# Optimization experiments

Measured on AMD Instinct MI355X. Metric: run time of the kernel, lower is better.

Reference implementation:

```python
import jax, jax.numpy as jnp
import numpy as np

EPS = 1e-5

def mean_variance_norm(x):
    # x: [b, c, h, w]; per-(b,c) instance norm over spatial, unbiased var (torch default)
    b, c, h, w = x.shape
    xf = x.reshape(b, c, h * w)
    mean = xf.mean(axis=2)
    var = xf.var(axis=2, ddof=1) + EPS
    std = jnp.sqrt(var)
    return (x - mean[:, :, None, None]) / std[:, :, None, None]

def conv1x1(x, w, b):
    # w: [out_c, in_c], b: [out_c]
    return jnp.einsum('oc,bchw->bohw', w, x) + b[None, :, None, None]

def setup_inputs() -> dict:
    key = jax.random.key(0)
    ks = jax.random.split(key, 10)
    b, C, H, W = 4, 512, 64, 64
    content = jax.random.normal(ks[0], (b, C, H, W), dtype=jnp.float32)
    style = jax.random.normal(ks[1], (b, C, H, W), dtype=jnp.float32)
    def w_(k, o, i):
        return jax.random.normal(k, (o, i), dtype=jnp.float32) * 0.02
    def b_(k, o):
        return jax.random.normal(k, (o,), dtype=jnp.float32) * 0.02
    return {
        'content': content, 'style': style,
        'f_w': w_(ks[2], C, C), 'f_b': b_(ks[3], C),
        'g_w': w_(ks[4], C, C), 'g_b': b_(ks[5], C),
        'h_w': w_(ks[6], C, C), 'h_b': b_(ks[7], C),
        'out_w': w_(ks[8], C, C), 'out_b': b_(ks[9], C),
    }

def reference(content, style, f_w, f_b, g_w, g_b, h_w, h_b, out_w, out_b):
    b, C, h, w = content.shape
    F = conv1x1(mean_variance_norm(content), f_w, f_b)   # [b,C,h,w]
    G = conv1x1(mean_variance_norm(style), g_w, g_b)     # [b,C,hg,wg]
    H = conv1x1(style, h_w, h_b)                          # [b,C,hg,wg]
    # spatial <= max_sample, so no subsampling branch
    Gf = G.reshape(b, C, -1)                              # [b,C,M]
    Hf = H.reshape(b, C, -1)                              # [b,C,M]
    Ff = F.reshape(b, C, -1)                              # [b,C,N]
    S = jnp.einsum('bcn,bcm->bnm', Ff, Gf)                # [b,N,M]
    S = jax.nn.softmax(S, axis=-1)
    styled = jnp.einsum('bcm,bnm->bcn', Hf, S)            # [b,C,N]
    styled = styled.reshape(b, C, h, w)
    return conv1x1(styled, out_w, out_b)
```

## Files before the change

### kernel.cpp

```cpp
#include <hip/hip_runtime.h>
#include <hip/hip_bf16.h>

typedef _Float16 f16;
typedef __attribute__((ext_vector_type(8))) _Float16 half8;
typedef __attribute__((ext_vector_type(4))) _Float16 half4;
typedef __attribute__((ext_vector_type(4))) float f32x4;

#define AS1 __attribute__((address_space(1)))
#define AS3 __attribute__((address_space(3)))

constexpr int CH  = 512;
constexpr int NSP = 4096;
constexpr int NB  = 4;

#define VM8  asm volatile("s_waitcnt vmcnt(8)"  ::: "memory")
#define VM0  asm volatile("s_waitcnt vmcnt(0)"  ::: "memory")
#define BARS do { __builtin_amdgcn_s_barrier(); asm volatile("" ::: "memory"); } while (0)

__device__ __forceinline__ void gload_lds16(const void* g, void* l) {
    __builtin_amdgcn_global_load_lds((const AS1 void*)g, (AS3 void*)l, 16, 0, 0);
}

__global__ void stats_kernel(const float* __restrict__ c_, const float* __restrict__ s_,
                             float* __restrict__ stats)
{
    int row = blockIdx.x;
    const float* p = ((row < NB*CH) ? c_ : s_) + (size_t)(row & (NB*CH - 1)) * NSP;
    float s = 0.f, ss = 0.f;
    for (int i = threadIdx.x; i < NSP/4; i += 256) {
        float4 v = ((const float4*)p)[i];
        s  += v.x + v.y + v.z + v.w;
        ss += v.x*v.x + v.y*v.y + v.z*v.z + v.w*v.w;
    }
    #pragma unroll
    for (int off = 32; off; off >>= 1) { s += __shfl_down(s, off); ss += __shfl_down(ss, off); }
    __shared__ float r1[4], r2[4];
    if ((threadIdx.x & 63) == 0) { r1[threadIdx.x >> 6] = s; r2[threadIdx.x >> 6] = ss; }
    __syncthreads();
    if (threadIdx.x == 0) {
        s = r1[0]+r1[1]+r1[2]+r1[3]; ss = r2[0]+r2[1]+r2[2]+r2[3];
        float mean = s * (1.f/NSP);
        float var  = (ss - (float)NSP*mean*mean) * (1.f/(NSP-1));
        int base = (row < NB*CH) ? 0 : 2*NB*CH;
        int r = row & (NB*CH - 1);
        stats[base + r] = mean;
        stats[base + NB*CH + r] = rsqrtf(var + 1e-5f);
    }
}

__global__ void effw_kernel(const float* __restrict__ fw, const float* __restrict__ fb,
                            const float* __restrict__ gw, const float* __restrict__ gb,
                            const float* __restrict__ hw, const float* __restrict__ ow,
                            const float* __restrict__ stats,
                            f16* __restrict__ fw_e, float* __restrict__ fb_e,
                            f16* __restrict__ gw_e, float* __restrict__ gb_e,
                            f16* __restrict__ hw_h, f16* __restrict__ ow_h)
{
    int o = blockIdx.x, b = blockIdx.y, mode = blockIdx.z, t = threadIdx.x;
    if (mode >= 2) {
        if (b != 0) return;
        const float* srcw = (mode == 2) ? hw : ow;
        f16* dstw = (mode == 2) ? hw_h : ow_h;
        for (int c = t; c < CH; c += 128) dstw[o*CH + c] = (f16)srcw[o*CH + c];
        return;
    }
    const float* w  = mode ? gw : fw;
    const float* st = stats + (mode ? 2*NB*CH : 0);
    f16* we = mode ? gw_e : fw_e;
    float part = 0.f;
    for (int c = t; c < CH; c += 128) {
        float mn = st[b*CH + c], is = st[NB*CH + b*CH + c];
        float wv = w[o*CH + c];
        we[((size_t)b*CH + o)*CH + c] = (f16)(wv * is);
        part += wv * mn * is;
    }
    #pragma unroll
    for (int off = 32; off; off >>= 1) part += __shfl_down(part, off);
    __shared__ float rr[2];
    if ((t & 63) == 0) rr[t >> 6] = part;
    __syncthreads();
    if (t == 0) (mode ? gb_e : fb_e)[b*CH + o] = (mode ? gb : fb)[o] - (rr[0] + rr[1]);
}

__global__ void transpose_f16_kernel(const float* __restrict__ content, const float* __restrict__ style,
                                     f16* __restrict__ content_t, f16* __restrict__ style_t)
{
    int b = blockIdx.z & 3, is_style = blockIdx.z >> 2;
    const float* src = (is_style ? style : content) + (size_t)b * CH * NSP;
    f16* dst = (is_style ? style_t : content_t) + (size_t)b * NSP * CH;
    int c0 = blockIdx.y * 64, n0 = blockIdx.x * 64;
    __shared__ f16 tile[64][72];
    int t = threadIdx.x;
    #pragma unroll
    for (int i = 0; i < 4; i++) {
        int idx = t + i*256;
        int cr = idx >> 4, n4 = (idx & 15) * 4;
        float4 v = *(const float4*)(src + (size_t)(c0+cr)*NSP + n0 + n4);
        tile[cr][n4+0] = (f16)v.x; tile[cr][n4+1] = (f16)v.y;
        tile[cr][n4+2] = (f16)v.z; tile[cr][n4+3] = (f16)v.w;
    }
    __syncthreads();
    int nr = t >> 2, seg = (t & 3) * 16;
    __align__(16) f16 out_v[16];
    #pragma unroll
    for (int j = 0; j < 16; j++) out_v[j] = tile[seg + j][nr];
    f16* dp = dst + (size_t)(n0+nr)*CH + c0 + seg;
    *(int4*)dp = ((int4*)out_v)[0];
    *(int4*)(dp + 8) = ((int4*)out_v)[1];
}

template<int MODE>
__global__ __launch_bounds__(256)
void gemm_kernel(const f16* __restrict__ W, long wstrideb,
                 const f16* __restrict__ Xt, long xstrideb,
                 const float* __restrict__ bias, long bstrideb,
                 void* __restrict__ Y, long ystrideb,
                 int K, long ostride)
{
    const int z = blockIdx.z;
    W    += (size_t)z * wstrideb;
    Xt   += (size_t)z * xstrideb;
    bias += (size_t)z * bstrideb;
    const int m0 = blockIdx.y * 128, n0 = blockIdx.x * 128;
    const int t = threadIdx.x, wave = t >> 6, lane = t & 63;
    const int l15 = lane & 15, l4 = lane >> 4;
    const int wm = (wave >> 1) * 64, wn = (wave & 1) * 64;

    __shared__ __align__(16) f16 Al[2][8192];
    __shared__ __align__(16) f16 Bl[2][8192];

    f32x4 acc[4][4] = {};

    auto stage = [&](int bufi, int kk) {
        #pragma unroll
        for (int j = 0; j < 4; j++) {
            int L  = ((wave*4 + j)*64 + lane) * 16;
            int SL = L ^ (((L >> 7) & 7) << 4);
            int row = SL >> 7, seg = (SL & 127) >> 1;
            gload_lds16(W  + (size_t)(m0 + row)*K + kk + seg, &Al[bufi][L >> 1]);
            gload_lds16(Xt + (size_t)(n0 + row)*K + kk + seg, &Bl[bufi][L >> 1]);
        }
    };

    const int nks = K >> 6;
    stage(0, 0);
    for (int ks = 0; ks < nks; ks++) {
        int bufi = ks & 1;
        if (ks < nks-1) { stage(bufi ^ 1, (ks + 1) * 64); VM8; }
        else            { VM0; }
        BARS;
        #pragma unroll
        for (int kb = 0; kb < 2; kb++) {
            half8 a[4], bb[4];
            #pragma unroll
            for (int i = 0; i < 4; i++) {
                int ab = (wm + i*16 + l15)*128 + kb*64 + l4*16;
                ab ^= ((ab >> 7) & 7) << 4;
                a[i] = *(const half8*)&Al[bufi][ab >> 1];
                int bby = (wn + i*16 + l15)*128 + kb*64 + l4*16;
                bby ^= ((bby >> 7) & 7) << 4;
                bb[i] = *(const half8*)&Bl[bufi][bby >> 1];
            }
            #pragma unroll
            for (int i = 0; i < 4; i++)
                #pragma unroll
                for (int jj = 0; jj < 4; jj++)
                    acc[i][jj] = __builtin_amdgcn_mfma_f32_16x16x32_f16(a[i], bb[jj], acc[i][jj], 0, 0, 0);
        }
        BARS;
    }

    #pragma unroll
    for (int i = 0; i < 4; i++) {
        const int ob = m0 + wm + i*16 + l4*4;
        f32x4 bv = *(const f32x4*)(bias + ob);
        #pragma unroll
        for (int jj = 0; jj < 4; jj++) {
            const int n = n0 + wn + jj*16 + l15;
            f32x4 v = acc[i][jj];
            v[0] += bv[0]; v[1] += bv[1]; v[2] += bv[2]; v[3] += bv[3];
            if constexpr (MODE == 0) {
                f16* Yb = (f16*)Y + (size_t)z * ystrideb;
                half4 pk; pk[0]=(f16)v[0]; pk[1]=(f16)v[1]; pk[2]=(f16)v[2]; pk[3]=(f16)v[3];
                *(half4*)(Yb + (size_t)n * ostride + ob) = pk;
            } else if constexpr (MODE == 1) {
                f16* Yb = (f16*)Y + (size_t)z * ystrideb;
                #pragma unroll
                for (int r = 0; r < 4; r++) Yb[(size_t)(ob + r) * ostride + n] = (f16)v[r];
            } else {
                float* Yf = (float*)Y + (size_t)z * ystrideb;
                #pragma unroll
                for (int r = 0; r < 4; r++) Yf[(size_t)(ob + r) * ostride + n] = v[r];
            }
        }
    }
}

__global__ __launch_bounds__(256)
void softmax_kernel(f16* __restrict__ S, int nrows)
{
    int row = blockIdx.x * 4 + (threadIdx.x >> 6);
    if (row >= nrows) return;
    int lane = threadIdx.x & 63;
    f16* p = S + (size_t)row * NSP + lane * 8;

    half8 v[8];
    #pragma unroll
    for (int j = 0; j < 8; j++) v[j] = *(const half8*)(p + j * 512);

    float mx = -1e30f;
    #pragma unroll
    for (int j = 0; j < 8; j++)
        #pragma unroll
        for (int e = 0; e < 8; e++) mx = fmaxf(mx, (float)v[j][e]);
    #pragma unroll
    for (int off = 32; off; off >>= 1) mx = fmaxf(mx, __shfl_xor(mx, off));

    float ex[64];
    float s = 0.f;
    #pragma unroll
    for (int j = 0; j < 8; j++)
        #pragma unroll
        for (int e = 0; e < 8; e++) {
            float x = __expf((float)v[j][e] - mx);
            ex[j*8 + e] = x; s += x;
        }
    #pragma unroll
    for (int off = 32; off; off >>= 1) s += __shfl_xor(s, off);
    float inv = 1.0f / s;

    #pragma unroll
    for (int j = 0; j < 8; j++) {
        half8 o;
        #pragma unroll
        for (int e = 0; e < 8; e++) o[e] = (f16)(ex[j*8 + e] * inv);
        *(half8*)(p + j * 512) = o;
    }
}

extern "C" void kernel_launch(void* const* d_in, const int* in_sizes, int n_in,
                              void* d_out, int out_size, void* d_ws, size_t ws_size,
                              hipStream_t stream)
{
    const float* content = (const float*)d_in[0];
    const float* style   = (const float*)d_in[1];
    const float* f_w = (const float*)d_in[2];
    const float* f_b = (const float*)d_in[3];
    const float* g_w = (const float*)d_in[4];
    const float* g_b = (const float*)d_in[5];
    const float* h_w = (const float*)d_in[6];
    const float* h_b = (const float*)d_in[7];
    const float* o_w = (const float*)d_in[8];
    const float* o_b = (const float*)d_in[9];

    char* ws = (char*)d_ws;
    size_t off = 0;
    auto alloc = [&](size_t bytes) -> void* {
        void* p = ws + off;
        off += (bytes + 255) & ~(size_t)255;
        return p;
    };
    float* stats = (float*)alloc(4 * NB*CH * 4);
    float* zeros = (float*)alloc(NSP * 4);
    f16* fw_e = (f16*)alloc((size_t)NB*CH*CH*2);
    f16* gw_e = (f16*)alloc((size_t)NB*CH*CH*2);
    f16* hw_h = (f16*)alloc((size_t)CH*CH*2);
    f16* ow_h = (f16*)alloc((size_t)CH*CH*2);
    float* fb_e = (float*)alloc((size_t)NB*CH*4);
    float* gb_e = (float*)alloc((size_t)NB*CH*4);
    f16* content_t = (f16*)alloc((size_t)NB*NSP*CH*2);
    f16* style_t   = (f16*)alloc((size_t)NB*NSP*CH*2);
    f16* F_t = (f16*)alloc((size_t)NB*NSP*CH*2);
    f16* G_t = (f16*)alloc((size_t)NB*NSP*CH*2);
    f16* H_  = (f16*)alloc((size_t)NB*CH*NSP*2);
    f16* styled_t = content_t;

    size_t s_plane = (size_t)NSP * NSP;
    bool all4 = (off + 4 * s_plane * 2 <= ws_size);
    f16* S16 = (f16*)alloc((all4 ? 4 : 1) * s_plane * 2);
    if (off > ws_size) return;

    hipMemsetAsync(zeros, 0, NSP * 4, stream);
    stats_kernel<<<dim3(2*NB*CH), dim3(256), 0, stream>>>(content, style, stats);
    effw_kernel<<<dim3(CH, NB, 4), dim3(128), 0, stream>>>(f_w, f_b, g_w, g_b, h_w, o_w, stats,
                                                           fw_e, fb_e, gw_e, gb_e, hw_h, ow_h);
    transpose_f16_kernel<<<dim3(NSP/64, CH/64, NB*2), dim3(256), 0, stream>>>(content, style, content_t, style_t);

    gemm_kernel<0><<<dim3(NSP/128, CH/128, NB), dim3(256), 0, stream>>>(
        fw_e, (long)CH*CH, content_t, (long)NSP*CH, fb_e, (long)CH, (void*)F_t, (long)NSP*CH, CH, (long)CH);
    gemm_kernel<0><<<dim3(NSP/128, CH/128, NB), dim3(256), 0, stream>>>(
        gw_e, (long)CH*CH, style_t, (long)NSP*CH, gb_e, (long)CH, (void*)G_t, (long)NSP*CH, CH, (long)CH);
    gemm_kernel<1><<<dim3(NSP/128, CH/128, NB), dim3(256), 0, stream>>>(
        hw_h, 0L, style_t, (long)NSP*CH, h_b, 0L, (void*)H_, (long)CH*NSP, CH, (long)NSP);

    if (all4) {
        gemm_kernel<0><<<dim3(NSP/128, NSP/128, NB), dim3(256), 0, stream>>>(
            G_t, (long)NSP*CH, F_t, (long)NSP*CH, zeros, 0L, (void*)S16, (long)s_plane, CH, (long)NSP);
        softmax_kernel<<<dim3(NB*NSP/4), dim3(256), 0, stream>>>(S16, NB*NSP);
        gemm_kernel<0><<<dim3(NSP/128, CH/128, NB), dim3(256), 0, stream>>>(
            H_, (long)CH*NSP, S16, (long)s_plane, zeros, 0L, (void*)styled_t, (long)NSP*CH, NSP, (long)CH);
    } else {
        for (int b = 0; b < NB; b++) {
            gemm_kernel<0><<<dim3(NSP/128, NSP/128, 1), dim3(256), 0, stream>>>(
                G_t + (size_t)b*NSP*CH, 0L, F_t + (size_t)b*NSP*CH, 0L, zeros, 0L,
                (void*)S16, 0L, CH, (long)NSP);
            softmax_kernel<<<dim3(NSP/4), dim3(256), 0, stream>>>(S16, NSP);
            gemm_kernel<0><<<dim3(NSP/128, CH/128, 1), dim3(256), 0, stream>>>(
                H_ + (size_t)b*CH*NSP, 0L, S16, 0L, zeros, 0L,
                (void*)(styled_t + (size_t)b*NSP*CH), 0L, NSP, (long)CH);
        }
    }

    gemm_kernel<2><<<dim3(NSP/128, CH/128, NB), dim3(256), 0, stream>>>(
        ow_h, 0L, styled_t, (long)NSP*CH, o_b, 0L, d_out, (long)CH*NSP, CH, (long)NSP);
}
```

Measured before the change: 343.7 us.

## Add 256x256-tile pipelined GEMM kernel for attention score and weighted-sum GEMMs

Adds a 512-thread GEMM kernel with 256x256 output tiles, double-buffered LDS filled by direct global-to-LDS loads, and a four-phase schedule that interleaves the next tile's loads with MFMA work using sched barriers and wave priority. It replaces the 128x128 GEMMs for the S=GᵀF product and the S·H product. The second GEMM swaps its operand roles so S becomes the M side with transposed output. The aim is more operand reuse per LDS load and better hiding of memory latency in the two largest GEMMs. In exchange it uses much more LDS and registers per block, which lowers occupancy, and the styled GEMM launches only 2 tiles along N per batch.

```diff
diff --git a/kernel.cpp b/kernel.cpp
--- a/kernel.cpp
+++ b/kernel.cpp
@@ -13,9 +13,13 @@
 constexpr int NSP = 4096;
 constexpr int NB  = 4;
 
+#define VMC2 asm volatile("s_waitcnt vmcnt(2)" ::: "memory")
 #define VM8  asm volatile("s_waitcnt vmcnt(8)"  ::: "memory")
 #define VM0  asm volatile("s_waitcnt vmcnt(0)"  ::: "memory")
 #define BARS do { __builtin_amdgcn_s_barrier(); asm volatile("" ::: "memory"); } while (0)
+#define SB0  __builtin_amdgcn_sched_barrier(0)
+#define SP1  __builtin_amdgcn_s_setprio(1)
+#define SP0  __builtin_amdgcn_s_setprio(0)
 
 __device__ __forceinline__ void gload_lds16(const void* g, void* l) {
     __builtin_amdgcn_global_load_lds((const AS1 void*)g, (AS3 void*)l, 16, 0, 0);
@@ -191,6 +195,136 @@
                 float* Yf = (float*)Y + (size_t)z * ystrideb;
                 #pragma unroll
                 for (int r = 0; r < 4; r++) Yf[(size_t)(ob + r) * ostride + n] = v[r];
+            }
+        }
+    }
+}
+
+template<int MODE>
+__global__ __launch_bounds__(512)
+void gemm256_kernel(const f16* __restrict__ W, long wstrideb,
+                    const f16* __restrict__ Xt, long xstrideb,
+                    void* __restrict__ Y, long ystrideb,
+                    int K, long ostride)
+{
+    const int z = blockIdx.z;
+    W  += (size_t)z * wstrideb;
+    Xt += (size_t)z * xstrideb;
+    const int m0 = blockIdx.y * 256, n0 = blockIdx.x * 256;
+    const int t = threadIdx.x, lane = t & 63;
+    const int wave = t >> 6;
+    const int l15 = lane & 15, l4 = lane >> 4;
+    const int wr = wave >> 2, wc = wave & 3;
+
+    __shared__ __align__(16) f16 As[2][16384];
+    __shared__ __align__(16) f16 Bs[2][16384];
+
+    f32x4 acc[8][4] = {};
+
+    auto stA = [&](int nbuf, int kk, int q) {
+        int L = q*8192 + t*16;
+        int SL = L ^ (((L >> 7) & 7) << 4);
+        gload_lds16(W + (size_t)(m0 + (SL >> 7))*K + kk + ((SL & 127) >> 1), &As[nbuf][L >> 1]);
+    };
+    auto stB = [&](int nbuf, int kk, int q) {
+        int L = q*8192 + t*16;
+        int SL = L ^ (((L >> 7) & 7) << 4);
+        gload_lds16(Xt + (size_t)(n0 + (SL >> 7))*K + kk + ((SL & 127) >> 1), &Bs[nbuf][L >> 1]);
+    };
+    auto ldA = [&](int buf, int i, int kb) {
+        int L = (wr*128 + i*16 + l15)*128 + kb*64 + l4*16;
+        L ^= ((L >> 7) & 7) << 4;
+        return *(const half8*)&As[buf][L >> 1];
+    };
+    auto ldB = [&](int buf, int j, int kb) {
+        int L = (wc*64 + j*16 + l15)*128 + kb*64 + l4*16;
+        L ^= ((L >> 7) & 7) << 4;
+        return *(const half8*)&Bs[buf][L >> 1];
+    };
+
+    const int nks = K >> 6;
+    #pragma unroll
+    for (int q = 0; q < 4; q++) stA(0, 0, q);
+    #pragma unroll
+    for (int q = 0; q < 4; q++) stB(0, 0, q);
+
+    half8 a[4][2], b01[2][2], b23[2][2];
+
+    for (int kt = 0; kt < nks; kt++) {
+        const int buf = kt & 1;
+        const bool st = (kt + 1 < nks);
+        const int kk1 = (kt + 1) << 6;
+
+        if (st) { stA(buf^1, kk1, 0); stA(buf^1, kk1, 1); VMC2; }
+        else    { VM0; }
+        BARS;
+        #pragma unroll
+        for (int i = 0; i < 4; i++) { a[i][0] = ldA(buf, i, 0); a[i][1] = ldA(buf, i, 1); }
+        #pragma unroll
+        for (int j = 0; j < 2; j++) { b01[j][0] = ldB(buf, j, 0); b01[j][1] = ldB(buf, j, 1); }
+        SB0; SP1;
+        #pragma unroll
+        for (int i = 0; i < 4; i++)
+            #pragma unroll
+            for (int j = 0; j < 2; j++)
+                #pragma unroll
+                for (int kb = 0; kb < 2; kb++)
+                    acc[i][j] = __builtin_amdgcn_mfma_f32_16x16x32_f16(a[i][kb], b01[j][kb], acc[i][j], 0, 0, 0);
+        SP0; SB0; BARS;
+
+        if (st) { stA(buf^1, kk1, 2); stA(buf^1, kk1, 3); }
+        #pragma unroll
+        for (int j = 0; j < 2; j++) { b23[j][0] = ldB(buf, 2+j, 0); b23[j][1] = ldB(buf, 2+j, 1); }
+        SB0; SP1;
+        #pragma unroll
+        for (int i = 0; i < 4; i++)
+            #pragma unroll
+            for (int j = 0; j < 2; j++)
+                #pragma unroll
+                for (int kb = 0; kb < 2; kb++)
+                    acc[i][2+j] = __builtin_amdgcn_mfma_f32_16x16x32_f16(a[i][kb], b23[j][kb], acc[i][2+j], 0, 0, 0);
+        SP0; SB0; BARS;
+
+        if (st) { stB(buf^1, kk1, 0); stB(buf^1, kk1, 1); }
+        #pragma unroll
+        for (int i = 0; i < 4; i++) { a[i][0] = ldA(buf, 4+i, 0); a[i][1] = ldA(buf, 4+i, 1); }
+        SB0; SP1;
+        #pragma unroll
+        for (int i = 0; i < 4; i++)
+            #pragma unroll
+            for (int j = 0; j < 2; j++)
+                #pragma unroll
+                for (int kb = 0; kb < 2; kb++)
+                    acc[4+i][2+j] = __builtin_amdgcn_mfma_f32_16x16x32_f16(a[i][kb], b23[j][kb], acc[4+i][2+j], 0, 0, 0);
+        SP0; SB0; BARS;
+
+        if (st) { stB(buf^1, kk1, 2); stB(buf^1, kk1, 3); }
+        SB0; SP1;
+        #pragma unroll
+        for (int i = 0; i < 4; i++)
+            #pragma unroll
+            for (int j = 0; j < 2; j++)
+                #pragma unroll
+                for (int kb = 0; kb < 2; kb++)
+                    acc[4+i][j] = __builtin_amdgcn_mfma_f32_16x16x32_f16(a[i][kb], b01[j][kb], acc[4+i][j], 0, 0, 0);
+        SP0; SB0; BARS;
+    }
+
+    #pragma unroll
+    for (int i = 0; i < 8; i++) {
+        const int ob = m0 + wr*128 + i*16 + l4*4;
+        #pragma unroll
+        for (int j = 0; j < 4; j++) {
+            const int ncol = n0 + wc*64 + j*16 + l15;
+            f32x4 v = acc[i][j];
+            if constexpr (MODE == 0) {
+                f16* Yb = (f16*)Y + (size_t)z * ystrideb;
+                half4 pk; pk[0]=(f16)v[0]; pk[1]=(f16)v[1]; pk[2]=(f16)v[2]; pk[3]=(f16)v[3];
+                *(half4*)(Yb + (size_t)ncol * ostride + ob) = pk;
+            } else {
+                f16* Yb = (f16*)Y + (size_t)z * ystrideb;
+                #pragma unroll
+                for (int r = 0; r < 4; r++) Yb[(size_t)(ob + r) * ostride + ncol] = (f16)v[r];
             }
         }
     }
@@ -294,19 +428,19 @@
         hw_h, 0L, style_t, (long)NSP*CH, h_b, 0L, (void*)H_, (long)CH*NSP, CH, (long)NSP);
 
     if (all4) {
-        gemm_kernel<0><<<dim3(NSP/128, NSP/128, NB), dim3(256), 0, stream>>>(
-            G_t, (long)NSP*CH, F_t, (long)NSP*CH, zeros, 0L, (void*)S16, (long)s_plane, CH, (long)NSP);
+        gemm256_kernel<0><<<dim3(NSP/256, NSP/256, NB), dim3(512), 0, stream>>>(
+            G_t, (long)NSP*CH, F_t, (long)NSP*CH, (void*)S16, (long)s_plane, CH, (long)NSP);
         softmax_kernel<<<dim3(NB*NSP/4), dim3(256), 0, stream>>>(S16, NB*NSP);
-        gemm_kernel<0><<<dim3(NSP/128, CH/128, NB), dim3(256), 0, stream>>>(
-            H_, (long)CH*NSP, S16, (long)s_plane, zeros, 0L, (void*)styled_t, (long)NSP*CH, NSP, (long)CH);
+        gemm256_kernel<1><<<dim3(CH/256, NSP/256, NB), dim3(512), 0, stream>>>(
+            S16, (long)s_plane, H_, (long)CH*NSP, (void*)styled_t, (long)NSP*CH, NSP, (long)CH);
     } else {
         for (int b = 0; b < NB; b++) {
-            gemm_kernel<0><<<dim3(NSP/128, NSP/128, 1), dim3(256), 0, stream>>>(
-                G_t + (size_t)b*NSP*CH, 0L, F_t + (size_t)b*NSP*CH, 0L, zeros, 0L,
+            gemm256_kernel<0><<<dim3(NSP/256, NSP/256, 1), dim3(512), 0, stream>>>(
+                G_t + (size_t)b*NSP*CH, 0L, F_t + (size_t)b*NSP*CH, 0L,
                 (void*)S16, 0L, CH, (long)NSP);
             softmax_kernel<<<dim3(NSP/4), dim3(256), 0, stream>>>(S16, NSP);
-            gemm_kernel<0><<<dim3(NSP/128, CH/128, 1), dim3(256), 0, stream>>>(
-                H_ + (size_t)b*CH*NSP, 0L, S16, 0L, zeros, 0L,
+            gemm256_kernel<1><<<dim3(CH/256, NSP/256, 1), dim3(512), 0, stream>>>(
+                S16, 0L, H_ + (size_t)b*CH*NSP, 0L,
                 (void*)(styled_t + (size_t)b*NSP*CH), 0L, NSP, (long)CH);
         }
     }
```

Measured after the change: 400.9 us. 16.6% more time.

## Add dedicated attention GEMM with swizzled block mapping and swapped operands

Applied to the files above, without the earlier changes.

Adds a specialized attention GEMM kernel that uses a 1D grid remapped across 8 groups (XCD-aware tile ordering) and drops the bias add. The S=F·G and styled GEMMs now swap operand roles so the output is written row-major per element rather than through the old packed-transposed path. The aim is better cache locality across chiplets and cheaper epilogues. The trade-off is that the new kernel loads with a single buffer and a full wait each k-step, and its scalar f16 stores may coalesce worse.

```diff
diff --git a/kernel.cpp b/kernel.cpp
--- a/kernel.cpp
+++ b/kernel.cpp
@@ -192,6 +192,81 @@
                 #pragma unroll
                 for (int r = 0; r < 4; r++) Yf[(size_t)(ob + r) * ostride + n] = v[r];
             }
+        }
+    }
+}
+
+template<int TPB, int NCT>
+__global__ __launch_bounds__(256)
+void gemm_att_kernel(const f16* __restrict__ W, long wstrideb,
+                     const f16* __restrict__ Xt, long xstrideb,
+                     f16* __restrict__ Y, long ystrideb,
+                     int K, long ostride)
+{
+    const int T = gridDim.x;
+    const int bid = blockIdx.x;
+    const int tile = (bid & 7) * (T >> 3) + (bid >> 3);
+    const int z = tile / TPB, rem = tile - z * TPB;
+    const int mt = rem / NCT, nt = rem - mt * NCT;
+    W  += (size_t)z * wstrideb;
+    Xt += (size_t)z * xstrideb;
+    f16* Yb = Y + (size_t)z * ystrideb;
+    const int m0 = mt * 128, n0 = nt * 128;
+
+    const int t = threadIdx.x, wave = t >> 6, lane = t & 63;
+    const int l15 = lane & 15, l4 = lane >> 4;
+    const int wm = (wave >> 1) * 64, wn = (wave & 1) * 64;
+
+    __shared__ __align__(16) f16 Al[8192];
+    __shared__ __align__(16) f16 Bl[8192];
+
+    f32x4 acc[4][4] = {};
+
+    auto stage = [&](int kk) {
+        #pragma unroll
+        for (int j = 0; j < 4; j++) {
+            int L  = ((wave*4 + j)*64 + lane) * 16;
+            int SL = L ^ (((L >> 7) & 7) << 4);
+            int row = SL >> 7, seg = (SL & 127) >> 1;
+            gload_lds16(W  + (size_t)(m0 + row)*K + kk + seg, &Al[L >> 1]);
+            gload_lds16(Xt + (size_t)(n0 + row)*K + kk + seg, &Bl[L >> 1]);
+        }
+    };
+
+    const int nks = K >> 6;
+    for (int ks = 0; ks < nks; ks++) {
+        stage(ks * 64);
+        VM0; BARS;
+        #pragma unroll
+        for (int kb = 0; kb < 2; kb++) {
+            half8 a[4], bb[4];
+            #pragma unroll
+            for (int i = 0; i < 4; i++) {
+                int ab = (wm + i*16 + l15)*128 + kb*64 + l4*16;
+                ab ^= ((ab >> 7) & 7) << 4;
+                a[i] = *(const half8*)&Al[ab >> 1];
+                int bby = (wn + i*16 + l15)*128 + kb*64 + l4*16;
+                bby ^= ((bby >> 7) & 7) << 4;
+                bb[i] = *(const half8*)&Bl[bby >> 1];
+            }
+            #pragma unroll
+            for (int i = 0; i < 4; i++)
+                #pragma unroll
+                for (int jj = 0; jj < 4; jj++)
+                    acc[i][jj] = __builtin_amdgcn_mfma_f32_16x16x32_f16(a[i], bb[jj], acc[i][jj], 0, 0, 0);
+        }
+        BARS;
+    }
+
+    #pragma unroll
+    for (int i = 0; i < 4; i++) {
+        const int ob = m0 + wm + i*16 + l4*4;
+        #pragma unroll
+        for (int jj = 0; jj < 4; jj++) {
+            const int ncol = n0 + wn + jj*16 + l15;
+            #pragma unroll
+            for (int r = 0; r < 4; r++)
+                Yb[(size_t)(ob + r) * ostride + ncol] = (f16)acc[i][jj][r];
         }
     }
 }
@@ -294,20 +369,20 @@
         hw_h, 0L, style_t, (long)NSP*CH, h_b, 0L, (void*)H_, (long)CH*NSP, CH, (long)NSP);
 
     if (all4) {
-        gemm_kernel<0><<<dim3(NSP/128, NSP/128, NB), dim3(256), 0, stream>>>(
-            G_t, (long)NSP*CH, F_t, (long)NSP*CH, zeros, 0L, (void*)S16, (long)s_plane, CH, (long)NSP);
+        gemm_att_kernel<1024,32><<<dim3(NB*1024), dim3(256), 0, stream>>>(
+            F_t, (long)NSP*CH, G_t, (long)NSP*CH, S16, (long)s_plane, CH, (long)NSP);
         softmax_kernel<<<dim3(NB*NSP/4), dim3(256), 0, stream>>>(S16, NB*NSP);
-        gemm_kernel<0><<<dim3(NSP/128, CH/128, NB), dim3(256), 0, stream>>>(
-            H_, (long)CH*NSP, S16, (long)s_plane, zeros, 0L, (void*)styled_t, (long)NSP*CH, NSP, (long)CH);
+        gemm_att_kernel<128,4><<<dim3(NB*128), dim3(256), 0, stream>>>(
+            S16, (long)s_plane, H_, (long)CH*NSP, styled_t, (long)NSP*CH, NSP, (long)CH);
     } else {
         for (int b = 0; b < NB; b++) {
-            gemm_kernel<0><<<dim3(NSP/128, NSP/128, 1), dim3(256), 0, stream>>>(
-                G_t + (size_t)b*NSP*CH, 0L, F_t + (size_t)b*NSP*CH, 0L, zeros, 0L,
-                (void*)S16, 0L, CH, (long)NSP);
+            gemm_att_kernel<1024,32><<<dim3(1024), dim3(256), 0, stream>>>(
+                F_t + (size_t)b*NSP*CH, 0L, G_t + (size_t)b*NSP*CH, 0L,
+                S16, 0L, CH, (long)NSP);
             softmax_kernel<<<dim3(NSP/4), dim3(256), 0, stream>>>(S16, NSP);
-            gemm_kernel<0><<<dim3(NSP/128, CH/128, 1), dim3(256), 0, stream>>>(
-                H_ + (size_t)b*CH*NSP, 0L, S16, 0L, zeros, 0L,
-                (void*)(styled_t + (size_t)b*NSP*CH), 0L, NSP, (long)CH);
+            gemm_att_kernel<128,4><<<dim3(128), dim3(256), 0, stream>>>(
+                S16, 0L, H_ + (size_t)b*CH*NSP, 0L,
+                styled_t + (size_t)b*NSP*CH, 0L, NSP, (long)CH);
         }
     }
 
```

New measurement: 320.5 us. -6.7%, faster.
